# Kernel tuning notes

Measured on AMD Instinct MI355X. Metric: run time of the kernel, lower is better.

Reference implementation:

```python
import jax, jax.numpy as jnp
import numpy as np

COLUMN_COUNT = 1024
CELLS_PER_COLUMN = 8
NUM_CELLS = COLUMN_COUNT * CELLS_PER_COLUMN  # 8192
ACTIVATION_THRESHOLD = 13.0
PERM_CONNECTED = 0.5
PERM_INC = 0.1
PERM_DEC = 0.1


def setup_inputs() -> dict:
    key = jax.random.key(0)
    k1, k2, k3, k4 = jax.random.split(key, 4)
    active_columns = (jax.random.uniform(k1, (COLUMN_COUNT,)) < 0.02).astype(jnp.float32)
    # dense permanence matrix in [0,1); ~half connected at threshold 0.5
    segment_weights = jax.random.uniform(k2, (NUM_CELLS, NUM_CELLS), dtype=jnp.float32)
    # sparse binary previous predictive / active cell states
    predictive_cells = (jax.random.uniform(k3, (NUM_CELLS,)) < 0.01).astype(jnp.float32)
    prev_active_cells = (jax.random.uniform(k4, (NUM_CELLS,)) < 0.01).astype(jnp.float32)
    return {
        "active_columns": active_columns,
        "segment_weights": segment_weights,
        "predictive_cells": predictive_cells,
        "prev_active_cells": prev_active_cells,
    }


def reference(active_columns, segment_weights, predictive_cells, prev_active_cells):
    # --- compute_activity (vectorized over columns; no python loop) ---
    col_pred = predictive_cells.reshape(COLUMN_COUNT, CELLS_PER_COLUMN)
    col_has_pred = col_pred.sum(axis=1) > 0                      # [C] bool
    active_mask = active_columns > 0                             # [C] bool
    # per active column: use its predictions if any, else burst (all ones)
    per_col = jnp.where(col_has_pred[:, None], col_pred, 1.0)    # [C, cells]
    new_active = (per_col * active_mask[:, None].astype(col_pred.dtype)).reshape(NUM_CELLS)

    connected = (segment_weights >= PERM_CONNECTED).astype(segment_weights.dtype)
    presyn = connected @ new_active                              # [N] dense matvec
    new_predictive = (presyn >= ACTIVATION_THRESHOLD).astype(segment_weights.dtype)

    # --- anomaly: fraction of active columns that were NOT predicted ---
    num_active = jnp.sum(active_mask)
    num_predicted = jnp.sum(active_mask & col_has_pred)
    anomaly = 1.0 - num_predicted.astype(jnp.float32) / jnp.maximum(num_active, 1).astype(jnp.float32)

    # --- learn: outer-product permanence update, skipped if no prev activity ---
    delta = PERM_INC * new_active[None, :] * prev_active_cells[:, None]          # [N,N]
    decay = (PERM_DEC * 0.1) * (1.0 - new_active[None, :]) * prev_active_cells[:, None]
    updated = jnp.clip(segment_weights + delta - decay, 0.0, 1.0)
    new_segment_weights = jnp.where(prev_active_cells.sum() > 0, updated, segment_weights)

    return (new_active, new_predictive, anomaly, new_segment_weights)
```

## Files before the change

### kernel.cpp

```cpp
#include <hip/hip_runtime.h>

#define NUM_CELLS 8192
#define COLS 1024

typedef float vf4 __attribute__((ext_vector_type(4)));
typedef vf4 uvf4 __attribute__((aligned(4)));

__global__ __launch_bounds__(1024) void prep_kernel(
    const float* __restrict__ act_cols, const float* __restrict__ pred,
    const float* __restrict__ prev, float* __restrict__ out,
    float* __restrict__ ws) {
  const int t = threadIdx.x;
  float p[8];
  float colsum = 0.f;
#pragma unroll
  for (int k = 0; k < 8; k++) { p[k] = pred[t * 8 + k]; colsum += p[k]; }
  const bool has_pred = colsum > 0.f;
  const bool active = act_cols[t] > 0.f;
#pragma unroll
  for (int k = 0; k < 8; k++)
    out[t * 8 + k] = active ? (has_pred ? p[k] : 1.f) : 0.f;

  float nA = active ? 1.f : 0.f;
  float nP = (active && has_pred) ? 1.f : 0.f;
  float ps = 0.f;
#pragma unroll
  for (int k = 0; k < 8; k++) ps += prev[t * 8 + k];

#pragma unroll
  for (int off = 32; off; off >>= 1) {
    nA += __shfl_down(nA, off);
    nP += __shfl_down(nP, off);
    ps += __shfl_down(ps, off);
  }
  __shared__ float sA[16], sP[16], sS[16];
  const int wid = t >> 6;
  if ((t & 63) == 0) { sA[wid] = nA; sP[wid] = nP; sS[wid] = ps; }
  __syncthreads();
  if (t == 0) {
    float a = 0.f, pp = 0.f, s = 0.f;
    for (int i = 0; i < 16; i++) { a += sA[i]; pp += sP[i]; s += sS[i]; }
    out[2 * NUM_CELLS] = 1.0f - pp / fmaxf(a, 1.0f);
    ws[0] = (s > 0.f) ? 1.f : 0.f;
  }
}

__global__ __launch_bounds__(256) void fused_kernel(
    const float* __restrict__ W, const float* __restrict__ prev,
    float* __restrict__ out, const float* __restrict__ ws) {
  const int row = blockIdx.x;
  const int t = threadIdx.x;
  const float coef = prev[row] * ws[0];
  const float4* __restrict__ Wrow = (const float4*)(W + (size_t)row * NUM_CELLS);
  const float4* __restrict__ A = (const float4*)out;
  uvf4* __restrict__ Wout = (uvf4*)(out + 2 * NUM_CELLS + 1 + (size_t)row * NUM_CELLS);

  float sum = 0.f;
  if (coef > 0.f) {
#pragma unroll
    for (int k = 0; k < 8; k++) {
      const int idx = k * 256 + t;
      const float4 w = Wrow[idx];
      const float4 a = A[idx];
      sum += ((w.x >= 0.5f) ? a.x : 0.f) + ((w.y >= 0.5f) ? a.y : 0.f) +
             ((w.z >= 0.5f) ? a.z : 0.f) + ((w.w >= 0.5f) ? a.w : 0.f);
      uvf4 u;
      u.x = fminf(fmaxf(w.x + ((a.x > 0.5f) ? 0.1f : -0.01f), 0.f), 1.f);
      u.y = fminf(fmaxf(w.y + ((a.y > 0.5f) ? 0.1f : -0.01f), 0.f), 1.f);
      u.z = fminf(fmaxf(w.z + ((a.z > 0.5f) ? 0.1f : -0.01f), 0.f), 1.f);
      u.w = fminf(fmaxf(w.w + ((a.w > 0.5f) ? 0.1f : -0.01f), 0.f), 1.f);
      Wout[idx] = u;
    }
  } else {
#pragma unroll
    for (int k = 0; k < 8; k++) {
      const int idx = k * 256 + t;
      const float4 w = Wrow[idx];
      const float4 a = A[idx];
      sum += ((w.x >= 0.5f) ? a.x : 0.f) + ((w.y >= 0.5f) ? a.y : 0.f) +
             ((w.z >= 0.5f) ? a.z : 0.f) + ((w.w >= 0.5f) ? a.w : 0.f);
      uvf4 u = {w.x, w.y, w.z, w.w};
      Wout[idx] = u;
    }
  }

#pragma unroll
  for (int off = 32; off; off >>= 1) sum += __shfl_down(sum, off);
  __shared__ float s[4];
  if ((t & 63) == 0) s[t >> 6] = sum;
  __syncthreads();
  if (t == 0) {
    const float tot = s[0] + s[1] + s[2] + s[3];
    out[NUM_CELLS + row] = (tot >= 13.0f) ? 1.f : 0.f;
  }
}

extern "C" void kernel_launch(void* const* d_in, const int* in_sizes, int n_in,
                              void* d_out, int out_size, void* d_ws, size_t ws_size,
                              hipStream_t stream) {
  const float* act_cols = (const float*)d_in[0];
  const float* W = (const float*)d_in[1];
  const float* pred = (const float*)d_in[2];
  const float* prev = (const float*)d_in[3];
  float* out = (float*)d_out;
  float* ws = (float*)d_ws;

  prep_kernel<<<1, 1024, 0, stream>>>(act_cols, pred, prev, out, ws);
  fused_kernel<<<NUM_CELLS, 256, 0, stream>>>(W, prev, out, ws);
}
```

Before: 438.8 us.

## Map one wavefront per row and use nontemporal loads/stores for weight streaming

```diff
diff --git a/kernel.cpp b/kernel.cpp
--- a/kernel.cpp
+++ b/kernel.cpp
@@ -11,21 +11,31 @@
     const float* __restrict__ prev, float* __restrict__ out,
     float* __restrict__ ws) {
   const int t = threadIdx.x;
-  float p[8];
-  float colsum = 0.f;
-#pragma unroll
-  for (int k = 0; k < 8; k++) { p[k] = pred[t * 8 + k]; colsum += p[k]; }
+  const vf4* __restrict__ pred4 = (const vf4*)pred;
+  const vf4* __restrict__ prev4 = (const vf4*)prev;
+
+  const vf4 p0 = pred4[t * 2 + 0];
+  const vf4 p1 = pred4[t * 2 + 1];
+  const vf4 q0 = prev4[t * 2 + 0];
+  const vf4 q1 = prev4[t * 2 + 1];
+
+  const float colsum = p0.x + p0.y + p0.z + p0.w + p1.x + p1.y + p1.z + p1.w;
   const bool has_pred = colsum > 0.f;
   const bool active = act_cols[t] > 0.f;
-#pragma unroll
-  for (int k = 0; k < 8; k++)
-    out[t * 8 + k] = active ? (has_pred ? p[k] : 1.f) : 0.f;
+
+  vf4 o0, o1;
+  if (active) {
+    if (has_pred) { o0 = p0; o1 = p1; }
+    else          { o0 = (vf4){1.f,1.f,1.f,1.f}; o1 = (vf4){1.f,1.f,1.f,1.f}; }
+  } else {
+    o0 = (vf4){0.f,0.f,0.f,0.f}; o1 = o0;
+  }
+  ((vf4*)out)[t * 2 + 0] = o0;
+  ((vf4*)out)[t * 2 + 1] = o1;
 
   float nA = active ? 1.f : 0.f;
   float nP = (active && has_pred) ? 1.f : 0.f;
-  float ps = 0.f;
-#pragma unroll
-  for (int k = 0; k < 8; k++) ps += prev[t * 8 + k];
+  float ps = q0.x + q0.y + q0.z + q0.w + q1.x + q1.y + q1.z + q1.w;
 
 #pragma unroll
   for (int off = 32; off; off >>= 1) {
@@ -48,51 +58,46 @@
 __global__ __launch_bounds__(256) void fused_kernel(
     const float* __restrict__ W, const float* __restrict__ prev,
     float* __restrict__ out, const float* __restrict__ ws) {
-  const int row = blockIdx.x;
-  const int t = threadIdx.x;
+  const int lane = threadIdx.x & 63;
+  const int row = (blockIdx.x << 2) | (threadIdx.x >> 6);
+
   const float coef = prev[row] * ws[0];
-  const float4* __restrict__ Wrow = (const float4*)(W + (size_t)row * NUM_CELLS);
-  const float4* __restrict__ A = (const float4*)out;
+  const vf4* __restrict__ Wrow = (const vf4*)(W + (size_t)row * NUM_CELLS);
+  const vf4* __restrict__ A = (const vf4*)out;
   uvf4* __restrict__ Wout = (uvf4*)(out + 2 * NUM_CELLS + 1 + (size_t)row * NUM_CELLS);
 
   float sum = 0.f;
   if (coef > 0.f) {
-#pragma unroll
-    for (int k = 0; k < 8; k++) {
-      const int idx = k * 256 + t;
-      const float4 w = Wrow[idx];
-      const float4 a = A[idx];
+#pragma unroll 8
+    for (int k = 0; k < 32; k++) {
+      const int idx = (k << 6) | lane;
+      const vf4 w = __builtin_nontemporal_load(&Wrow[idx]);
+      const vf4 a = A[idx];
       sum += ((w.x >= 0.5f) ? a.x : 0.f) + ((w.y >= 0.5f) ? a.y : 0.f) +
              ((w.z >= 0.5f) ? a.z : 0.f) + ((w.w >= 0.5f) ? a.w : 0.f);
-      uvf4 u;
+      vf4 u;
       u.x = fminf(fmaxf(w.x + ((a.x > 0.5f) ? 0.1f : -0.01f), 0.f), 1.f);
       u.y = fminf(fmaxf(w.y + ((a.y > 0.5f) ? 0.1f : -0.01f), 0.f), 1.f);
       u.z = fminf(fmaxf(w.z + ((a.z > 0.5f) ? 0.1f : -0.01f), 0.f), 1.f);
       u.w = fminf(fmaxf(w.w + ((a.w > 0.5f) ? 0.1f : -0.01f), 0.f), 1.f);
-      Wout[idx] = u;
+      __builtin_nontemporal_store(u, &Wout[idx]);
     }
   } else {
-#pragma unroll
-    for (int k = 0; k < 8; k++) {
-      const int idx = k * 256 + t;
-      const float4 w = Wrow[idx];
-      const float4 a = A[idx];
+#pragma unroll 8
+    for (int k = 0; k < 32; k++) {
+      const int idx = (k << 6) | lane;
+      const vf4 w = __builtin_nontemporal_load(&Wrow[idx]);
+      const vf4 a = A[idx];
       sum += ((w.x >= 0.5f) ? a.x : 0.f) + ((w.y >= 0.5f) ? a.y : 0.f) +
              ((w.z >= 0.5f) ? a.z : 0.f) + ((w.w >= 0.5f) ? a.w : 0.f);
-      uvf4 u = {w.x, w.y, w.z, w.w};
-      Wout[idx] = u;
+      __builtin_nontemporal_store(w, &Wout[idx]);
     }
   }
 
 #pragma unroll
   for (int off = 32; off; off >>= 1) sum += __shfl_down(sum, off);
-  __shared__ float s[4];
-  if ((t & 63) == 0) s[t >> 6] = sum;
-  __syncthreads();
-  if (t == 0) {
-    const float tot = s[0] + s[1] + s[2] + s[3];
-    out[NUM_CELLS + row] = (tot >= 13.0f) ? 1.f : 0.f;
-  }
+  if (lane == 0)
+    out[NUM_CELLS + row] = (sum >= 13.0f) ? 1.f : 0.f;
 }
 
 extern "C" void kernel_launch(void* const* d_in, const int* in_sizes, int n_in,
@@ -106,5 +111,5 @@
   float* ws = (float*)d_ws;
 
   prep_kernel<<<1, 1024, 0, stream>>>(act_cols, pred, prev, out, ws);
-  fused_kernel<<<NUM_CELLS, 256, 0, stream>>>(W, prev, out, ws);
+  fused_kernel<<<NUM_CELLS / 4, 256, 0, stream>>>(W, prev, out, ws);
 }
```

Result: slower. 457.8 us (+4.3%).
